# Optimization experiments

Hardware: AMD Instinct MI355X
Metric: run time of the kernel (lower is better)

The kernel has to match this reference:

```python
import jax, jax.numpy as jnp
import numpy as np

NUM_USERS = 150000
NUM_ITEMS = 80000
N_NODES = NUM_USERS + NUM_ITEMS
NNZ = 5000000
LATENT_DIM = 64
N_LAYERS = 3


def setup_inputs() -> dict:
    key = jax.random.key(0)
    k1, k2, k3, k4, k5 = jax.random.split(key, 5)
    user_emb = 0.1 * jax.random.normal(k1, (NUM_USERS, LATENT_DIM), dtype=jnp.float32)
    item_emb = 0.1 * jax.random.normal(k2, (NUM_ITEMS, LATENT_DIM), dtype=jnp.float32)
    adj_rows = jax.random.randint(k3, (NNZ,), 0, N_NODES, dtype=jnp.int32)
    adj_cols = jax.random.randint(k4, (NNZ,), 0, N_NODES, dtype=jnp.int32)
    # scale values ~ 1/avg_degree so propagation is stable (mimics sym-normalized adjacency)
    adj_vals = jax.random.uniform(k5, (NNZ,), dtype=jnp.float32) * (N_NODES / NNZ)
    return {"user_emb": user_emb, "item_emb": item_emb,
            "adj_rows": adj_rows, "adj_cols": adj_cols, "adj_vals": adj_vals}


def _spmm(rows, cols, vals, x):
    # y[r] = sum_{e: rows[e]==r} vals[e] * x[cols[e]]  == torch.sparse.mm(G, x)
    return jax.ops.segment_sum(vals[:, None] * x[cols], rows, num_segments=N_NODES)


def reference(user_emb, item_emb, adj_rows, adj_cols, adj_vals):
    all_emb = jnp.concatenate([user_emb, item_emb], axis=0)  # [N, d]
    acc = all_emb
    for _ in range(N_LAYERS):
        all_emb = _spmm(adj_rows, adj_cols, adj_vals, all_emb)
        acc = acc + all_emb
    light_out = acc / (N_LAYERS + 1)  # mean over stacked layer embeddings
    users = light_out[:NUM_USERS]
    items = light_out[NUM_USERS:]
    return users, items
```

## Files before the change

kernel.cpp:

```cpp
#include <hip/hip_runtime.h>

#define NUM_USERS 150000
#define NUM_ITEMS 80000
#define N_NODES   230000
#define NNZ       5000000
#define DIM       64

#define SB_SHIFT 9
#define SB_SIZE  512
#define NUM_SB   ((N_NODES + SB_SIZE - 1) / SB_SIZE)
#define SB_CAP   12288
#define PA_ITEMS 8

#define NSLICES   (N_NODES / 8)

#define VAL_MAX   0.046f
#define VAL_ENC   (16384.0f / VAL_MAX)
#define VAL_SCALE (VAL_MAX / 16384.0f)

typedef int          i4 __attribute__((ext_vector_type(4)));
typedef float        f4 __attribute__((ext_vector_type(4)));
typedef unsigned int u4 __attribute__((ext_vector_type(4)));

__device__ __forceinline__ unsigned short f2bf(float f) {
    unsigned int u = __float_as_uint(f);
    u += 0x7FFFu + ((u >> 16) & 1u);
    return (unsigned short)(u >> 16);
}
__device__ __forceinline__ float bflo(unsigned int u) {
    return __uint_as_float(u << 16);
}
__device__ __forceinline__ float bfhi(unsigned int u) {
    return __uint_as_float(u & 0xFFFF0000u);
}
__device__ __forceinline__ unsigned int pk2(float a, float b) {
    return (unsigned int)f2bf(a) | ((unsigned int)f2bf(b) << 16);
}

__global__ void init_kernel(const float* __restrict__ u,
                            const float* __restrict__ it,
                            unsigned short* __restrict__ x,
                            int* __restrict__ bucket_cursor) {
    long i = (long)blockIdx.x * blockDim.x + threadIdx.x;
    if (i < NUM_SB) bucket_cursor[i] = 0;
    const long n4  = (long)N_NODES * DIM / 4;
    const long iu4 = (long)NUM_USERS * DIM / 4;
    if (i >= n4) return;
    f4 v = (i < iu4) ? __builtin_nontemporal_load((const f4*)u + i)
                     : __builtin_nontemporal_load((const f4*)it + (i - iu4));
    ushort4 h;
    h.x = f2bf(v[0]); h.y = f2bf(v[1]); h.z = f2bf(v[2]); h.w = f2bf(v[3]);
    ((ushort4*)x)[i] = h;
}

__global__ __launch_bounds__(1024)
void partA_kernel(const int* __restrict__ rows,
                  const int* __restrict__ cols,
                  const float* __restrict__ vals,
                  int* __restrict__ bucket_cursor,
                  uint2* __restrict__ Xu) {
    __shared__ int bcnt[NUM_SB];
    __shared__ int bbase[NUM_SB];
    const int t = threadIdx.x;
    const long tile = 1024L * PA_ITEMS;
    for (long base = (long)blockIdx.x * tile; base < NNZ;
         base += (long)gridDim.x * tile) {
        for (int j = t; j < NUM_SB; j += 1024) bcnt[j] = 0;
        __syncthreads();
        const long e0 = base + (long)t * PA_ITEMS;
        const bool ok = (e0 < NNZ);
        unsigned int pk[PA_ITEMS];
        int br[PA_ITEMS];
        if (ok) {
            const i4 r0 = __builtin_nontemporal_load((const i4*)(rows + e0));
            const i4 r1 = __builtin_nontemporal_load((const i4*)(rows + e0) + 1);
            const i4 c0 = __builtin_nontemporal_load((const i4*)(cols + e0));
            const i4 c1 = __builtin_nontemporal_load((const i4*)(cols + e0) + 1);
            const f4 v0 = __builtin_nontemporal_load((const f4*)(vals + e0));
            const f4 v1 = __builtin_nontemporal_load((const f4*)(vals + e0) + 1);
            const int   rr[8] = {r0[0], r0[1], r0[2], r0[3],
                                 r1[0], r1[1], r1[2], r1[3]};
            const int   cc[8] = {c0[0], c0[1], c0[2], c0[3],
                                 c1[0], c1[1], c1[2], c1[3]};
            const float vv[8] = {v0[0], v0[1], v0[2], v0[3],
                                 v1[0], v1[1], v1[2], v1[3]};
            #pragma unroll
            for (int k = 0; k < PA_ITEMS; ++k) {
                const int b  = rr[k] >> SB_SHIFT;
                const int rl = rr[k] & (SB_SIZE - 1);
                int vc = (int)(vv[k] * VAL_ENC + 0.5f);
                vc = min(vc, 16383);
                pk[k] = ((unsigned int)vc << 18) | (unsigned int)cc[k];
                const int rank = atomicAdd(&bcnt[b], 1);
                br[k] = (b << 22) | (rank << 9) | rl;
            }
        }
        __syncthreads();
        for (int j = t; j < NUM_SB; j += 1024)
            if (bcnt[j] > 0) {
                const int old = atomicAdd(&bucket_cursor[j], bcnt[j]);
                bbase[j] = j * SB_CAP + old;
            }
        __syncthreads();
        if (ok) {
            #pragma unroll
            for (int k = 0; k < PA_ITEMS; ++k) {
                const int b    = br[k] >> 22;
                const int rank = (br[k] >> 9) & 0x1FFF;
                const int rl   = br[k] & (SB_SIZE - 1);
                Xu[bbase[b] + rank] = make_uint2(pk[k], (unsigned int)rl);
            }
        }
        __syncthreads();
    }
}

__global__ __launch_bounds__(1024)
void partB_kernel(const uint2* __restrict__ Xu,
                  const int* __restrict__ bucket_cursor,
                  int* __restrict__ row_start,
                  unsigned int* __restrict__ edges) {
    __shared__ int bsc[512];
    __shared__ int hist[SB_SIZE];
    __shared__ int scn[SB_SIZE];
    const int b    = blockIdx.x;
    const int t    = threadIdx.x;
    const int rlo  = b << SB_SHIFT;
    const int nrows = min(SB_SIZE, N_NODES - rlo);
    const int xoff = b * SB_CAP;

    if (t < 512) bsc[t] = (t < NUM_SB) ? bucket_cursor[t] : 0;
    if (t < SB_SIZE) hist[t] = 0;
    __syncthreads();
    for (int off = 1; off < 512; off <<= 1) {
        int add = (t >= off && t < 512) ? bsc[t - off] : 0;
        __syncthreads();
        if (t < 512) bsc[t] += add;
        __syncthreads();
    }
    const int base = (b == 0) ? 0 : bsc[b - 1];
    const int cnt  = bsc[b] - base;

    for (int i = t; i < cnt; i += 1024)
        atomicAdd(&hist[Xu[xoff + i].y], 1);
    __syncthreads();
    const int v = (t < SB_SIZE) ? hist[t] : 0;
    if (t < SB_SIZE) scn[t] = v;
    __syncthreads();
    for (int off = 1; off < SB_SIZE; off <<= 1) {
        int add = (t >= off && t < SB_SIZE) ? scn[t - off] : 0;
        __syncthreads();
        if (t < SB_SIZE) scn[t] += add;
        __syncthreads();
    }
    if (t < SB_SIZE) {
        const int rs = base + (scn[t] - v);
        if (t < nrows) row_start[rlo + t] = rs;
        hist[t] = rs;
    }
    __syncthreads();
    for (int i = t; i < cnt; i += 1024) {
        const uint2 xu = Xu[xoff + i];
        const int pos = atomicAdd(&hist[xu.y], 1);
        edges[pos] = xu.x;
    }
    if (b == 0 && t == 0) row_start[N_NODES] = NNZ;
}

#define FMA8(v, h) \
    a0 = fmaf((v), bflo((h).x), a0); a1 = fmaf((v), bfhi((h).x), a1); \
    a2 = fmaf((v), bflo((h).y), a2); a3 = fmaf((v), bfhi((h).y), a3); \
    a4 = fmaf((v), bflo((h).z), a4); a5 = fmaf((v), bfhi((h).z), a5); \
    a6 = fmaf((v), bflo((h).w), a6); a7 = fmaf((v), bfhi((h).w), a7);

__global__ __launch_bounds__(256)
void spmm8_kernel(const int* __restrict__ row_start,
                  const unsigned int* __restrict__ edges,
                  const unsigned short* __restrict__ x,
                  unsigned short* __restrict__ y) {
    const int lane = threadIdx.x & 63;
    const int oct  = lane >> 3;
    const int fo   = (lane & 7) << 3;
    const int wv   = blockIdx.x * 4 + (threadIdx.x >> 6);
    if (wv >= NSLICES) return;
    const int row = wv * 8 + oct;
    const int s   = row_start[row];
    const int deg = row_start[row + 1] - s;
    int dm = deg;
    dm = max(dm, __shfl_xor(dm, 8));
    dm = max(dm, __shfl_xor(dm, 16));
    dm = max(dm, __shfl_xor(dm, 32));
    dm = __builtin_amdgcn_readfirstlane(dm);
    const unsigned short* xf = x + fo;
    float a0 = 0, a1 = 0, a2 = 0, a3 = 0, a4 = 0, a5 = 0, a6 = 0, a7 = 0;
    for (int i = 0; i < dm; i += 8) {
        unsigned int ev[8];
        uint4 h[8];
        #pragma unroll
        for (int k = 0; k < 8; ++k) {
            const int o = (i + k < deg) ? (s + i + k) : 0;
            ev[k] = edges[o];
        }
        #pragma unroll
        for (int k = 0; k < 8; ++k)
            h[k] = *(const uint4*)(xf + (((long)(ev[k] & 0x3FFFF)) << 6));
        #pragma unroll
        for (int k = 0; k < 8; ++k) {
            const float v = (i + k < deg)
                          ? (float)(ev[k] >> 18) * VAL_SCALE : 0.0f;
            FMA8(v, h[k]);
        }
    }
    u4 w;
    w[0] = pk2(a0, a1); w[1] = pk2(a2, a3);
    w[2] = pk2(a4, a5); w[3] = pk2(a6, a7);
    __builtin_nontemporal_store(w, (u4*)(y + (((long)row) << 6) + fo));
}

__global__ __launch_bounds__(256)
void spmm_final8_kernel(const int* __restrict__ row_start,
                        const unsigned int* __restrict__ edges,
                        const unsigned short* __restrict__ y2,
                        const unsigned short* __restrict__ y1,
                        const float* __restrict__ u,
                        const float* __restrict__ it,
                        float* __restrict__ acc) {
    const int lane = threadIdx.x & 63;
    const int oct  = lane >> 3;
    const int fo   = (lane & 7) << 3;
    const int wv   = blockIdx.x * 4 + (threadIdx.x >> 6);
    if (wv >= NSLICES) return;
    const int row = wv * 8 + oct;
    const int s   = row_start[row];
    const int deg = row_start[row + 1] - s;
    int dm = deg;
    dm = max(dm, __shfl_xor(dm, 8));
    dm = max(dm, __shfl_xor(dm, 16));
    dm = max(dm, __shfl_xor(dm, 32));
    dm = __builtin_amdgcn_readfirstlane(dm);
    const unsigned short* xf = y2 + fo;
    float a0 = 0, a1 = 0, a2 = 0, a3 = 0, a4 = 0, a5 = 0, a6 = 0, a7 = 0;
    for (int i = 0; i < dm; i += 8) {
        unsigned int ev[8];
        uint4 h[8];
        #pragma unroll
        for (int k = 0; k < 8; ++k) {
            const int o = (i + k < deg) ? (s + i + k) : 0;
            ev[k] = edges[o];
        }
        #pragma unroll
        for (int k = 0; k < 8; ++k)
            h[k] = *(const uint4*)(xf + (((long)(ev[k] & 0x3FFFF)) << 6));
        #pragma unroll
        for (int k = 0; k < 8; ++k) {
            const float v = (i + k < deg)
                          ? (float)(ev[k] >> 18) * VAL_SCALE : 0.0f;
            FMA8(v, h[k]);
        }
    }
    const long o = (((long)row) << 6) + fo;
    const float* x0p = (row < NUM_USERS) ? (u + o)
                     : (it + o - (((long)NUM_USERS) << 6));
    const f4 xa = __builtin_nontemporal_load((const f4*)x0p);
    const f4 xb = __builtin_nontemporal_load((const f4*)x0p + 1);
    const u4 h1 = __builtin_nontemporal_load((const u4*)(y1 + o));
    const uint4 h2 = *(const uint4*)(y2 + o);
    f4 ra, rb;
    ra[0] = (xa[0] + bflo(h1[0]) + bflo(h2.x) + a0) * 0.25f;
    ra[1] = (xa[1] + bfhi(h1[0]) + bfhi(h2.x) + a1) * 0.25f;
    ra[2] = (xa[2] + bflo(h1[1]) + bflo(h2.y) + a2) * 0.25f;
    ra[3] = (xa[3] + bfhi(h1[1]) + bfhi(h2.y) + a3) * 0.25f;
    rb[0] = (xb[0] + bflo(h1[2]) + bflo(h2.z) + a4) * 0.25f;
    rb[1] = (xb[1] + bfhi(h1[2]) + bfhi(h2.z) + a5) * 0.25f;
    rb[2] = (xb[2] + bflo(h1[3]) + bflo(h2.w) + a6) * 0.25f;
    rb[3] = (xb[3] + bfhi(h1[3]) + bfhi(h2.w) + a7) * 0.25f;
    __builtin_nontemporal_store(ra, (f4*)(acc + o));
    __builtin_nontemporal_store(rb, (f4*)(acc + o) + 1);
}

extern "C" void kernel_launch(void* const* d_in, const int* in_sizes, int n_in,
                              void* d_out, int out_size, void* d_ws, size_t ws_size,
                              hipStream_t stream) {
    const float* u    = (const float*)d_in[0];
    const float* it   = (const float*)d_in[1];
    const int*   rows = (const int*)d_in[2];
    const int*   cols = (const int*)d_in[3];
    const float* vals = (const float*)d_in[4];
    float* acc = (float*)d_out;

    const size_t bufBf = (size_t)N_NODES * DIM * 2;
    const size_t edgeB = (size_t)NNZ * 4;
    const size_t XuB   = (size_t)NUM_SB * SB_CAP * 8;
    const size_t nodeB = 921600;
    char* ws = (char*)d_ws;
    unsigned short* buf0 = (unsigned short*)(ws);
    unsigned short* buf1 = (unsigned short*)(ws + bufBf);
    unsigned short* buf2 = (unsigned short*)(ws + 2 * bufBf);
    unsigned int*   edges = (unsigned int*)(ws + 3 * bufBf);
    uint2*          Xu   = (uint2*)(ws + 3 * bufBf + edgeB);
    char* p              = ws + 3 * bufBf + edgeB + XuB;
    int* row_start       = (int*)(p);   p += nodeB;
    int* bucket_cursor   = (int*)(p);

    const int n4 = N_NODES * DIM / 4;
    const int ewGrid = (n4 + 255) / 256;

    init_kernel<<<ewGrid, 256, 0, stream>>>(u, it, buf0, bucket_cursor);

    partA_kernel<<<512, 1024, 0, stream>>>(rows, cols, vals, bucket_cursor, Xu);
    partB_kernel<<<NUM_SB, 1024, 0, stream>>>(Xu, bucket_cursor,
                                              row_start, edges);

    const int spmmGrid = (NSLICES + 3) / 4;
    spmm8_kernel<<<spmmGrid, 256, 0, stream>>>(row_start, edges, buf0, buf1);
    spmm8_kernel<<<spmmGrid, 256, 0, stream>>>(row_start, edges, buf1, buf2);
    spmm_final8_kernel<<<spmmGrid, 256, 0, stream>>>(row_start, edges, buf2,
                                                     buf1, u, it, acc);
}
```

Baseline: 505.3 us.

## Restructure bucket partition: one tile per block, defer col/val loads, precompute bucket scan

The partition kernel now processes exactly one 16-item tile per block instead of grid-striding, and loads cols/vals only after the shared-memory rank atomics so those loads overlap the global cursor atomics. The per-superbucket prefix scan that every partB block used to recompute is moved into a small single-block kernel that writes bucket bases once. This is meant to cut redundant scan work and latency in the preprocessing stages, at the cost of one extra kernel launch and more registers per thread.

```diff
diff --git a/kernel.cpp b/kernel.cpp
--- a/kernel.cpp
+++ b/kernel.cpp
@@ -10,7 +10,9 @@
 #define SB_SIZE  512
 #define NUM_SB   ((N_NODES + SB_SIZE - 1) / SB_SIZE)
 #define SB_CAP   12288
-#define PA_ITEMS 8
+#define PA_ITEMS 16
+#define PA_TILE  (1024 * PA_ITEMS)
+#define PA_GRID  ((NNZ + PA_TILE - 1) / PA_TILE)
 
 #define NSLICES   (N_NODES / 8)
 
@@ -62,65 +64,87 @@
     __shared__ int bcnt[NUM_SB];
     __shared__ int bbase[NUM_SB];
     const int t = threadIdx.x;
-    const long tile = 1024L * PA_ITEMS;
-    for (long base = (long)blockIdx.x * tile; base < NNZ;
-         base += (long)gridDim.x * tile) {
-        for (int j = t; j < NUM_SB; j += 1024) bcnt[j] = 0;
+    const long base = (long)blockIdx.x * PA_TILE;
+    for (int j = t; j < NUM_SB; j += 1024) bcnt[j] = 0;
+    __syncthreads();
+    const long e0 = base + (long)t * PA_ITEMS;
+    const bool ok = (e0 < NNZ);
+    unsigned int br[PA_ITEMS];
+    if (ok) {
+        const i4 r0 = __builtin_nontemporal_load((const i4*)(rows + e0));
+        const i4 r1 = __builtin_nontemporal_load((const i4*)(rows + e0) + 1);
+        const i4 r2 = __builtin_nontemporal_load((const i4*)(rows + e0) + 2);
+        const i4 r3 = __builtin_nontemporal_load((const i4*)(rows + e0) + 3);
+        const int rr[16] = {r0[0], r0[1], r0[2], r0[3], r1[0], r1[1], r1[2], r1[3],
+                            r2[0], r2[1], r2[2], r2[3], r3[0], r3[1], r3[2], r3[3]};
+        #pragma unroll
+        for (int k = 0; k < PA_ITEMS; ++k) {
+            const int b  = rr[k] >> SB_SHIFT;
+            const int rl = rr[k] & (SB_SIZE - 1);
+            const unsigned int rank = (unsigned int)atomicAdd(&bcnt[b], 1);
+            br[k] = (rank << 18) | ((unsigned int)b << 9) | (unsigned int)rl;
+        }
+    }
+    __syncthreads();
+    i4 c0 = {}, c1 = {}, c2 = {}, c3 = {};
+    f4 v0 = {}, v1 = {}, v2 = {}, v3 = {};
+    if (ok) {
+        c0 = __builtin_nontemporal_load((const i4*)(cols + e0));
+        c1 = __builtin_nontemporal_load((const i4*)(cols + e0) + 1);
+        c2 = __builtin_nontemporal_load((const i4*)(cols + e0) + 2);
+        c3 = __builtin_nontemporal_load((const i4*)(cols + e0) + 3);
+        v0 = __builtin_nontemporal_load((const f4*)(vals + e0));
+        v1 = __builtin_nontemporal_load((const f4*)(vals + e0) + 1);
+        v2 = __builtin_nontemporal_load((const f4*)(vals + e0) + 2);
+        v3 = __builtin_nontemporal_load((const f4*)(vals + e0) + 3);
+    }
+    for (int j = t; j < NUM_SB; j += 1024)
+        if (bcnt[j] > 0) {
+            const int old = atomicAdd(&bucket_cursor[j], bcnt[j]);
+            bbase[j] = j * SB_CAP + old;
+        }
+    __syncthreads();
+    if (ok) {
+        const int   cc[16] = {c0[0], c0[1], c0[2], c0[3], c1[0], c1[1], c1[2], c1[3],
+                              c2[0], c2[1], c2[2], c2[3], c3[0], c3[1], c3[2], c3[3]};
+        const float vv[16] = {v0[0], v0[1], v0[2], v0[3], v1[0], v1[1], v1[2], v1[3],
+                              v2[0], v2[1], v2[2], v2[3], v3[0], v3[1], v3[2], v3[3]};
+        #pragma unroll
+        for (int k = 0; k < PA_ITEMS; ++k) {
+            const int rank = (int)(br[k] >> 18);
+            const int b    = (int)((br[k] >> 9) & 0x1FF);
+            const int rl   = (int)(br[k] & 0x1FF);
+            int vc = (int)(vv[k] * VAL_ENC + 0.5f);
+            vc = min(vc, 16383);
+            const unsigned int pk =
+                ((unsigned int)vc << 18) | (unsigned int)cc[k];
+            Xu[bbase[b] + rank] = make_uint2(pk, (unsigned int)rl);
+        }
+    }
+}
+
+__global__ void sb_scan_kernel(const int* __restrict__ bucket_cursor,
+                               int* __restrict__ sb_base) {
+    __shared__ int lds[512];
+    const int t = threadIdx.x;
+    const int s = (t < NUM_SB) ? bucket_cursor[t] : 0;
+    lds[t] = s;
+    __syncthreads();
+    for (int off = 1; off < 512; off <<= 1) {
+        int add = (t >= off) ? lds[t - off] : 0;
         __syncthreads();
-        const long e0 = base + (long)t * PA_ITEMS;
-        const bool ok = (e0 < NNZ);
-        unsigned int pk[PA_ITEMS];
-        int br[PA_ITEMS];
-        if (ok) {
-            const i4 r0 = __builtin_nontemporal_load((const i4*)(rows + e0));
-            const i4 r1 = __builtin_nontemporal_load((const i4*)(rows + e0) + 1);
-            const i4 c0 = __builtin_nontemporal_load((const i4*)(cols + e0));
-            const i4 c1 = __builtin_nontemporal_load((const i4*)(cols + e0) + 1);
-            const f4 v0 = __builtin_nontemporal_load((const f4*)(vals + e0));
-            const f4 v1 = __builtin_nontemporal_load((const f4*)(vals + e0) + 1);
-            const int   rr[8] = {r0[0], r0[1], r0[2], r0[3],
-                                 r1[0], r1[1], r1[2], r1[3]};
-            const int   cc[8] = {c0[0], c0[1], c0[2], c0[3],
-                                 c1[0], c1[1], c1[2], c1[3]};
-            const float vv[8] = {v0[0], v0[1], v0[2], v0[3],
-                                 v1[0], v1[1], v1[2], v1[3]};
-            #pragma unroll
-            for (int k = 0; k < PA_ITEMS; ++k) {
-                const int b  = rr[k] >> SB_SHIFT;
-                const int rl = rr[k] & (SB_SIZE - 1);
-                int vc = (int)(vv[k] * VAL_ENC + 0.5f);
-                vc = min(vc, 16383);
-                pk[k] = ((unsigned int)vc << 18) | (unsigned int)cc[k];
-                const int rank = atomicAdd(&bcnt[b], 1);
-                br[k] = (b << 22) | (rank << 9) | rl;
-            }
-        }
+        lds[t] += add;
         __syncthreads();
-        for (int j = t; j < NUM_SB; j += 1024)
-            if (bcnt[j] > 0) {
-                const int old = atomicAdd(&bucket_cursor[j], bcnt[j]);
-                bbase[j] = j * SB_CAP + old;
-            }
-        __syncthreads();
-        if (ok) {
-            #pragma unroll
-            for (int k = 0; k < PA_ITEMS; ++k) {
-                const int b    = br[k] >> 22;
-                const int rank = (br[k] >> 9) & 0x1FFF;
-                const int rl   = br[k] & (SB_SIZE - 1);
-                Xu[bbase[b] + rank] = make_uint2(pk[k], (unsigned int)rl);
-            }
-        }
-        __syncthreads();
-    }
+    }
+    if (t < NUM_SB) sb_base[t] = lds[t] - s;
+    if (t == 0) sb_base[NUM_SB] = NNZ;
 }
 
 __global__ __launch_bounds__(1024)
 void partB_kernel(const uint2* __restrict__ Xu,
-                  const int* __restrict__ bucket_cursor,
+                  const int* __restrict__ sb_base,
                   int* __restrict__ row_start,
                   unsigned int* __restrict__ edges) {
-    __shared__ int bsc[512];
     __shared__ int hist[SB_SIZE];
     __shared__ int scn[SB_SIZE];
     const int b    = blockIdx.x;
@@ -128,19 +152,10 @@
     const int rlo  = b << SB_SHIFT;
     const int nrows = min(SB_SIZE, N_NODES - rlo);
     const int xoff = b * SB_CAP;
-
-    if (t < 512) bsc[t] = (t < NUM_SB) ? bucket_cursor[t] : 0;
+    const int base = sb_base[b];
+    const int cnt  = sb_base[b + 1] - base;
     if (t < SB_SIZE) hist[t] = 0;
     __syncthreads();
-    for (int off = 1; off < 512; off <<= 1) {
-        int add = (t >= off && t < 512) ? bsc[t - off] : 0;
-        __syncthreads();
-        if (t < 512) bsc[t] += add;
-        __syncthreads();
-    }
-    const int base = (b == 0) ? 0 : bsc[b - 1];
-    const int cnt  = bsc[b] - base;
-
     for (int i = t; i < cnt; i += 1024)
         atomicAdd(&hist[Xu[xoff + i].y], 1);
     __syncthreads();
@@ -300,16 +315,18 @@
     uint2*          Xu   = (uint2*)(ws + 3 * bufBf + edgeB);
     char* p              = ws + 3 * bufBf + edgeB + XuB;
     int* row_start       = (int*)(p);   p += nodeB;
-    int* bucket_cursor   = (int*)(p);
+    int* bucket_cursor   = (int*)(p);   p += 4096;
+    int* sb_base         = (int*)(p);
 
     const int n4 = N_NODES * DIM / 4;
     const int ewGrid = (n4 + 255) / 256;
 
     init_kernel<<<ewGrid, 256, 0, stream>>>(u, it, buf0, bucket_cursor);
 
-    partA_kernel<<<512, 1024, 0, stream>>>(rows, cols, vals, bucket_cursor, Xu);
-    partB_kernel<<<NUM_SB, 1024, 0, stream>>>(Xu, bucket_cursor,
-                                              row_start, edges);
+    partA_kernel<<<PA_GRID, 1024, 0, stream>>>(rows, cols, vals,
+                                               bucket_cursor, Xu);
+    sb_scan_kernel<<<1, 512, 0, stream>>>(bucket_cursor, sb_base);
+    partB_kernel<<<NUM_SB, 1024, 0, stream>>>(Xu, sb_base, row_start, edges);
 
     const int spmmGrid = (NSLICES + 3) / 4;
     spmm8_kernel<<<spmmGrid, 256, 0, stream>>>(row_start, edges, buf0, buf1);
```

New measurement: 520.2 us. 1.03x slower.
